# Kernel tuning notes

Hardware: AMD Instinct MI355X
Metric: run time of the kernel (lower is better)

The kernel has to match this reference:

```python
import jax, jax.numpy as jnp
import numpy as np
import math

EMBED = 1024
HEADS = 16
HEAD_DIM = EMBED // HEADS


def setup_inputs() -> dict:
    key = jax.random.key(0)
    ks = jax.random.split(key, 9)
    B, S = 2, 2048
    query = jax.random.normal(ks[0], (B, S, EMBED), dtype=jnp.float32)
    key_t = jax.random.normal(ks[1], (B, S, EMBED), dtype=jnp.float32)
    value = jax.random.normal(ks[2], (B, S, EMBED), dtype=jnp.float32)
    mask = jax.random.randint(ks[3], (B, 1, S, S), 0, 2, dtype=jnp.int32)
    # nn.Linear(head_dim, head_dim, bias=False) weights: [out, in]
    sc = 1.0 / math.sqrt(HEAD_DIM)
    Wq = jax.random.uniform(ks[4], (HEAD_DIM, HEAD_DIM), jnp.float32, -sc, sc)
    Wk = jax.random.uniform(ks[5], (HEAD_DIM, HEAD_DIM), jnp.float32, -sc, sc)
    Wv = jax.random.uniform(ks[6], (HEAD_DIM, HEAD_DIM), jnp.float32, -sc, sc)
    so = 1.0 / math.sqrt(EMBED)
    Wo = jax.random.uniform(ks[7], (EMBED, EMBED), jnp.float32, -so, so)
    bo = jax.random.uniform(ks[8], (EMBED,), jnp.float32, -so, so)
    return {"query": query, "key": key_t, "value": value, "mask": mask,
            "Wq": Wq, "Wk": Wk, "Wv": Wv, "Wo": Wo, "bo": bo}


def reference(query, key, value, mask, Wq, Wk, Wv, Wo, bo):
    B, Sq, E = query.shape
    Sk = key.shape[1]
    H, D = HEADS, HEAD_DIM
    # Faithful raw reshape into heads (as in the torch source, no transpose)
    q = query.reshape(B, H, Sq, D)
    k = key.reshape(B, H, Sk, D)
    v = value.reshape(B, H, Sk, D)
    # per-head_dim Linear (bias-free): x @ W.T
    Q = jnp.einsum('bhsd,ed->bhse', q, Wq)
    K = jnp.einsum('bhsd,ed->bhse', k, Wk)
    V = jnp.einsum('bhsd,ed->bhse', v, Wv)
    scores = jnp.einsum('bhqd,bhkd->bhqk', Q, K)  # [B,H,Sq,Sk]
    scores = jnp.where(mask == 0, jnp.float32(-1e20), scores)
    # NOTE: source divides by sqrt(embed_size), not sqrt(head_dim)
    attn = jax.nn.softmax(scores / jnp.float32(math.sqrt(E)), axis=-1)
    out = jnp.einsum('bhqk,bhkd->bhqd', attn, V).reshape(B, Sq, H * D)
    return out @ Wo.T + bo
```

## Files before the change

### kernel.cpp

```cpp
#include <hip/hip_runtime.h>

typedef __attribute__((ext_vector_type(8))) short short8;
typedef __attribute__((ext_vector_type(4))) float f32x4;
typedef __attribute__((ext_vector_type(2))) int int2v;
typedef __attribute__((ext_vector_type(4))) int int4v;

__device__ __forceinline__ short f2bf(float f) {
  unsigned u = __builtin_bit_cast(unsigned, f);
  u += 0x7fff + ((u >> 16) & 1);
  return (short)(u >> 16);
}

__device__ __forceinline__ int pk2bf(float lo, float hi) {
#if defined(__gfx950__) && __has_builtin(__builtin_amdgcn_cvt_pk_bf16_f32)
  typedef __attribute__((ext_vector_type(2))) __bf16 bf16x2;
  bf16x2 v = __builtin_amdgcn_cvt_pk_bf16_f32(lo, hi);
  return __builtin_bit_cast(int, v);
#else
  return (int)(unsigned short)(short)f2bf(lo) | (((int)f2bf(hi)) << 16);
#endif
}

__device__ __forceinline__ short8 pack8(f32x4 a, f32x4 b) {
  int4v t;
  t.x = pk2bf(a[0], a[1]);
  t.y = pk2bf(a[2], a[3]);
  t.z = pk2bf(b[0], b[1]);
  t.w = pk2bf(b[2], b[3]);
  return __builtin_bit_cast(short8, t);
}

__device__ __forceinline__ float fand(float p, int m) {
  return __builtin_bit_cast(float, __builtin_bit_cast(int, p) & m);
}

__device__ __forceinline__ float fexp2(float x) {
#if __has_builtin(__builtin_amdgcn_exp2f)
  return __builtin_amdgcn_exp2f(x);
#else
  return exp2f(x);
#endif
}

__device__ __forceinline__ float bf2f(short s) {
  return __builtin_bit_cast(float, ((int)(unsigned short)s) << 16);
}

__device__ __forceinline__ void glds16(const short* g, short* lbase, int lane) {
#if __has_builtin(__builtin_amdgcn_global_load_lds)
  __builtin_amdgcn_global_load_lds(
      (const __attribute__((address_space(1))) unsigned int*)g,
      (__attribute__((address_space(3))) unsigned int*)lbase, 16, 0, 0);
#else
  *(short8*)(lbase + lane * 8) = *(const short8*)g;
#endif
}

__global__ __launch_bounds__(256) void prep(const float* __restrict__ q,
                                            const float* __restrict__ k,
                                            const float* __restrict__ v,
                                            const float* __restrict__ Wq,
                                            const float* __restrict__ Wk,
                                            const float* __restrict__ Wv,
                                            const float* __restrict__ Wo,
                                            const int* __restrict__ mask,
                                            short* __restrict__ Qp,
                                            short* __restrict__ Kp,
                                            short* __restrict__ Vtp,
                                            short* __restrict__ Wob,
                                            unsigned* __restrict__ mmod) {
  const int bid = blockIdx.x;
  const int tid = threadIdx.x;

  if (bid >= 4096) {
    const int mb = bid - 4096;
    const int kp = mb & 15, bq = mb >> 4;
    const int b_ = bq >> 5, q64 = bq & 31;
    const int wv = tid >> 6, qd = (tid >> 4) & 3, m16_ = tid & 15;
    unsigned d = 0;
#pragma unroll
    for (int hb = 0; hb < 2; ++hb) {
      const int ka = kp * 2 + hb;
#pragma unroll
      for (int r = 0; r < 4; ++r) {
        const int* mr = mask + b_ * 4194304 +
                        (q64 * 64 + wv * 16 + qd * 4 + r) * 2048 + ka * 64 + m16_;
#pragma unroll
        for (int nt = 0; nt < 4; ++nt)
          if (mr[nt * 16] != 0) d |= 1u << (hb * 16 + r * 4 + nt);
      }
    }
    mmod[mb * 256 + tid] = d;
    return;
  }
  if (bid >= 3072) {
    const int i = ((bid - 3072) * 256 + tid) * 4;
    const f32x4 x = *(const f32x4*)&Wo[i];
    int2v o;
    o.x = pk2bf(x[0], x[1]);
    o.y = pk2bf(x[2], x[3]);
    *(int2v*)&Wob[i] = o;
    return;
  }

  __shared__ short xt[64][72];
  __shared__ short ot[64][72];
  const int mode = bid >> 10;
  const int bt = bid & 1023;
  const float* X;
  const float* W;
  float scale;
  if (mode == 0) { X = q; W = Wq; scale = 0.045084220f; }
  else if (mode == 1) { X = k; W = Wk; scale = 1.0f; }
  else { X = v; W = Wv; scale = 1.0f; }

  const int r0 = bt * 64;
  const int row = tid >> 2, seg = (tid & 3) * 16;
  const f32x4* xs = (const f32x4*)(X + (r0 + row) * 64 + seg);
  const f32x4 x0 = xs[0], x1 = xs[1], x2 = xs[2], x3 = xs[3];
  *(short8*)&xt[row][seg] = pack8(x0, x1);
  *(short8*)&xt[row][seg + 8] = pack8(x2, x3);
  __syncthreads();

  const int lane = tid & 63, wave = tid >> 6;
  const int m16 = lane & 15, quad = lane >> 4;

  const short8 a0 = *(const short8*)&xt[wave * 16 + m16][quad * 8];
  const short8 a1 = *(const short8*)&xt[wave * 16 + m16][32 + quad * 8];

  f32x4 acc[4];
#pragma unroll
  for (int nt = 0; nt < 4; ++nt) {
    const f32x4* wp0 = (const f32x4*)&W[(nt * 16 + m16) * 64 + quad * 8];
    const f32x4* wp1 = (const f32x4*)&W[(nt * 16 + m16) * 64 + 32 + quad * 8];
    const short8 b0 = pack8(wp0[0], wp0[1]);
    const short8 b1 = pack8(wp1[0], wp1[1]);
    f32x4 z = (f32x4){0.f, 0.f, 0.f, 0.f};
    z = __builtin_amdgcn_mfma_f32_16x16x32_bf16(a0, b0, z, 0, 0, 0);
    z = __builtin_amdgcn_mfma_f32_16x16x32_bf16(a1, b1, z, 0, 0, 0);
    acc[nt] = z;
  }

  if (mode != 2) {
#pragma unroll
    for (int nt = 0; nt < 4; ++nt)
#pragma unroll
      for (int r = 0; r < 4; ++r)
        ot[wave * 16 + quad * 4 + r][nt * 16 + m16] = f2bf(acc[nt][r] * scale);
  } else {
#pragma unroll
    for (int nt = 0; nt < 4; ++nt)
#pragma unroll
      for (int r = 0; r < 4; ++r)
        ot[nt * 16 + m16][16 * quad + 4 * r + wave] = f2bf(acc[nt][r]);
  }
  __syncthreads();

  const int orow = tid >> 2, opart = tid & 3;
  if (mode != 2) {
    short* dst = (mode == 0 ? Qp : Kp) + (r0 + orow) * 64 + opart * 16;
    *(short8*)&dst[0] = *(const short8*)&ot[orow][opart * 16];
    *(short8*)&dst[8] = *(const short8*)&ot[orow][opart * 16 + 8];
  } else {
    const int bh = r0 >> 11, s0 = r0 & 2047;
    short* dst = Vtp + bh * 131072 + orow * 2048 + s0 + opart * 16;
    *(short8*)&dst[0] = *(const short8*)&ot[orow][opart * 16];
    *(short8*)&dst[8] = *(const short8*)&ot[orow][opart * 16 + 8];
  }
}

__global__ __launch_bounds__(256, 4) void flash64s(const short* __restrict__ Qp,
                                                   const short* __restrict__ Kp,
                                                   const short* __restrict__ Vt,
                                                   const unsigned* __restrict__ mmod,
                                                   short* __restrict__ Opart,
                                                   float* __restrict__ lpart) {
  __shared__ __attribute__((aligned(16))) short kt[4096];
  __shared__ __attribute__((aligned(16))) short vt[4096];
  __shared__ __attribute__((aligned(16))) short pt[64][72];
  const int tid = threadIdx.x;
  const int bid = blockIdx.x;
  const int local = bid >> 3;
  const int khalf = local & 1;
  const int qblk = (local >> 1) & 31;
  const int bh = (bid & 7) * 4 + (local >> 6);
  const int q0 = qblk << 6;
  const int b = bh >> 4;
  const short* Qh = Qp + bh * 131072;
  const short* Kh = Kp + bh * 131072;
  const short* Vh = Vt + bh * 131072;
  const int lane = tid & 63, wave = tid >> 6;
  const int m16 = lane & 15, quad = lane >> 4;
  const int srow = lane >> 3, sj = (lane & 7) ^ srow;
  const int msh = m16 * 4;
  const int koff = m16 * 128 + ((quad ^ (m16 & 7)) * 16);

  const unsigned* mq = mmod + ((b * 32 + qblk) * 16 + khalf * 8) * 256 + tid;
  unsigned mw8[8];
#pragma unroll
  for (int kk = 0; kk < 8; ++kk) mw8[kk] = mq[kk * 256];

  short8 aq[2];
#pragma unroll
  for (int h = 0; h < 2; ++h)
    aq[h] = *(const short8*)&Qh[(q0 + wave * 16 + m16) * 64 + h * 32 + quad * 8];

  float l[4] = {0.f, 0.f, 0.f, 0.f};
  f32x4 oacc[4];
#pragma unroll
  for (int dt = 0; dt < 4; ++dt) oacc[dt] = (f32x4){0.f, 0.f, 0.f, 0.f};

  const int ka0 = khalf * 16;
  for (int kk = 0; kk < 8; ++kk) {
#pragma unroll
    for (int h = 0; h < 2; ++h) {
      const int ka = ka0 + kk * 2 + h;
      const int k0 = ka << 6;
      __syncthreads();
#pragma unroll
      for (int t = 0; t < 2; ++t) {
        const int crow = wave * 16 + t * 8;
        glds16(Kh + (ka * 64 + crow + srow) * 64 + sj * 8, kt + crow * 64, lane);
        glds16(Vh + (crow + srow) * 2048 + k0 + sj * 8, vt + crow * 64, lane);
      }
      __syncthreads();

      f32x4 s[4];
#pragma unroll
      for (int nt = 0; nt < 4; ++nt) {
        const int o0 = nt * 2048 + koff;
        const short8 kb0 = *(const short8*)((const char*)kt + o0);
        const short8 kb1 = *(const short8*)((const char*)kt + (o0 ^ 64));
        f32x4 z = (f32x4){0.f, 0.f, 0.f, 0.f};
        z = __builtin_amdgcn_mfma_f32_16x16x32_bf16(aq[0], kb0, z, 0, 0, 0);
        z = __builtin_amdgcn_mfma_f32_16x16x32_bf16(aq[1], kb1, z, 0, 0, 0);
        s[nt] = z;
      }

      const unsigned mw = mw8[kk];
      const int bitbase = h * 16;
#pragma unroll
      for (int r = 0; r < 4; ++r) {
        float p[4];
#pragma unroll
        for (int nt = 0; nt < 4; ++nt) {
          const int sh = 31 - (bitbase + r * 4 + nt);
          const int m = ((int)(mw << sh)) >> 31;
          p[nt] = fand(fexp2(s[nt][r]), m);
        }
        l[r] += (p[0] + p[1]) + (p[2] + p[3]);
        int2v pp;
        pp.x = pk2bf(p[0], p[1]);
        pp.y = pk2bf(p[2], p[3]);
        *(int2v*)&pt[wave * 16 + quad * 4 + r][msh] = pp;
      }

      const short8 ap0 = *(const short8*)&pt[wave * 16 + m16][quad * 8];
      const short8 ap1 = *(const short8*)&pt[wave * 16 + m16][32 + quad * 8];
#pragma unroll
      for (int dt = 0; dt < 4; ++dt) {
        const int o0 = dt * 2048 + koff;
        const short8 vb0 = *(const short8*)((const char*)vt + o0);
        const short8 vb1 = *(const short8*)((const char*)vt + (o0 ^ 64));
        f32x4 z = oacc[dt];
        z = __builtin_amdgcn_mfma_f32_16x16x32_bf16(ap0, vb0, z, 0, 0, 0);
        z = __builtin_amdgcn_mfma_f32_16x16x32_bf16(ap1, vb1, z, 0, 0, 0);
        oacc[dt] = z;
      }
    }
  }

  short* Oh = Opart + khalf * 4194304;
  float* lh = lpart + khalf * 65536;
#pragma unroll
  for (int r = 0; r < 4; ++r) {
#pragma unroll
    for (int off = 1; off < 16; off <<= 1) l[r] += __shfl_xor(l[r], off, 16);
    const float inv = 1.0f / l[r];
#pragma unroll
    for (int dt = 0; dt < 4; ++dt)
      pt[wave * 16 + quad * 4 + r][dt * 16 + m16] = f2bf(oacc[dt][r] * inv);
    if (m16 == 0) lh[bh * 2048 + q0 + wave * 16 + quad * 4 + r] = l[r];
  }

  const int orow = lane >> 2, opart = lane & 3;
  const int prow = wave * 16 + orow;
  short* og = Oh + (bh * 2048 + q0 + prow) * 64 + opart * 16;
  *(short8*)&og[0] = *(const short8*)&pt[prow][opart * 16];
  *(short8*)&og[8] = *(const short8*)&pt[prow][opart * 16 + 8];
}

__global__ __launch_bounds__(256) void outproj(const short* __restrict__ O0,
                                               const short* __restrict__ O1,
                                               const float* __restrict__ lp,
                                               const short* __restrict__ Wob,
                                               const float* __restrict__ bo,
                                               float* __restrict__ out) {
  __shared__ short at[64][72];
  __shared__ short bt[128][72];
  const int tid = threadIdx.x;
  const int bid = blockIdx.x;
  const int ct = bid >> 6, rt = bid & 63;
  const int r0 = rt * 64, c0 = ct * 128;
  const int lane = tid & 63, wave = tid >> 6;
  const int mr = (wave >> 1) * 32, nc = (wave & 1) * 64;
  const int m16 = lane & 15, quad = lane >> 4;
  const int arow = tid >> 2, apart = tid & 3;
  const int brow = tid >> 1, bhalf = (tid & 1) * 32;
  const int rr = r0 + arow;
  const int lbase = (rr >> 7) * 2048 + (rr & 127) * 16;

  f32x4 acc[2][4];
#pragma unroll
  for (int mt = 0; mt < 2; ++mt)
#pragma unroll
    for (int nt = 0; nt < 4; ++nt) acc[mt][nt] = (f32x4){0.f, 0.f, 0.f, 0.f};

  for (int kc = 0; kc < 16; ++kc) {
    const float l1 = lp[lbase + kc], l2 = lp[65536 + lbase + kc];
    const float is = 1.0f / (l1 + l2);
    const float w1 = l1 * is, w2 = l2 * is;
    const short8 a0 = *(const short8*)&O0[rr * 1024 + kc * 64 + apart * 16];
    const short8 a1 = *(const short8*)&O1[rr * 1024 + kc * 64 + apart * 16];
    const short8 a0b = *(const short8*)&O0[rr * 1024 + kc * 64 + apart * 16 + 8];
    const short8 a1b = *(const short8*)&O1[rr * 1024 + kc * 64 + apart * 16 + 8];
    const short* bg = &Wob[(c0 + brow) * 1024 + kc * 64 + bhalf];
    __syncthreads();
    int4v ca, cb;
    float f[8];
#pragma unroll
    for (int j = 0; j < 8; ++j) f[j] = w1 * bf2f(a0[j]) + w2 * bf2f(a1[j]);
    ca.x = pk2bf(f[0], f[1]); ca.y = pk2bf(f[2], f[3]);
    ca.z = pk2bf(f[4], f[5]); ca.w = pk2bf(f[6], f[7]);
#pragma unroll
    for (int j = 0; j < 8; ++j) f[j] = w1 * bf2f(a0b[j]) + w2 * bf2f(a1b[j]);
    cb.x = pk2bf(f[0], f[1]); cb.y = pk2bf(f[2], f[3]);
    cb.z = pk2bf(f[4], f[5]); cb.w = pk2bf(f[6], f[7]);
    *(short8*)&at[arow][apart * 16] = __builtin_bit_cast(short8, ca);
    *(short8*)&at[arow][apart * 16 + 8] = __builtin_bit_cast(short8, cb);
    *(short8*)&bt[brow][bhalf] = *(const short8*)&bg[0];
    *(short8*)&bt[brow][bhalf + 8] = *(const short8*)&bg[8];
    *(short8*)&bt[brow][bhalf + 16] = *(const short8*)&bg[16];
    *(short8*)&bt[brow][bhalf + 24] = *(const short8*)&bg[24];
    __syncthreads();

#pragma unroll
    for (int kh = 0; kh < 2; ++kh) {
      short8 af[2], bf[4];
#pragma unroll
      for (int i = 0; i < 2; ++i)
        af[i] = *(const short8*)&at[mr + i * 16 + m16][kh * 32 + quad * 8];
#pragma unroll
      for (int j = 0; j < 4; ++j)
        bf[j] = *(const short8*)&bt[nc + j * 16 + m16][kh * 32 + quad * 8];
#pragma unroll
      for (int mt = 0; mt < 2; ++mt)
#pragma unroll
        for (int nt = 0; nt < 4; ++nt)
          acc[mt][nt] = __builtin_amdgcn_mfma_f32_16x16x32_bf16(af[mt], bf[nt], acc[mt][nt], 0, 0, 0);
    }
  }

#pragma unroll
  for (int nt = 0; nt < 4; ++nt) {
    const int col = c0 + nc + nt * 16 + m16;
    const float bias = bo[col];
#pragma unroll
    for (int mt = 0; mt < 2; ++mt)
#pragma unroll
      for (int rr2 = 0; rr2 < 4; ++rr2)
        out[(r0 + mr + mt * 16 + quad * 4 + rr2) * 1024 + col] = acc[mt][nt][rr2] + bias;
  }
}

extern "C" void kernel_launch(void* const* d_in, const int* in_sizes, int n_in,
                              void* d_out, int out_size, void* d_ws, size_t ws_size,
                              hipStream_t stream) {
  const float* query = (const float*)d_in[0];
  const float* key = (const float*)d_in[1];
  const float* value = (const float*)d_in[2];
  const int* mask = (const int*)d_in[3];
  const float* Wq = (const float*)d_in[4];
  const float* Wk = (const float*)d_in[5];
  const float* Wv = (const float*)d_in[6];
  const float* Wo = (const float*)d_in[7];
  const float* bo = (const float*)d_in[8];
  float* out = (float*)d_out;

  char* ws = (char*)d_ws;
  short* Qp = (short*)(ws);
  short* Kp = (short*)(ws + 8388608);
  short* Vt = (short*)(ws + 16777216);
  short* Opart = (short*)(ws + 25165824);
  short* Wob = (short*)(ws + 41943040);
  float* lp = (float*)(ws + 44040192);
  unsigned* mmod = (unsigned*)(ws + 44564480);

  prep<<<5120, 256, 0, stream>>>(query, key, value, Wq, Wk, Wv, Wo, mask,
                                 Qp, Kp, Vt, Wob, mmod);
  flash64s<<<2048, 256, 0, stream>>>(Qp, Kp, Vt, mmod, Opart, lp);
  outproj<<<512, 256, 0, stream>>>(Opart, Opart + 4194304, lp, Wob, bo, out);
}
```

Baseline: 240.6 us.

## Enlarge flash attention query tile to 128 rows per block for K/V reuse

The attention kernel now handles 128 query rows per block, with each wave owning two 16-row groups, so every K/V tile staged in shared memory feeds twice as many MFMAs and the grid halves to 1024 blocks. The mask words and Q fragments are loaded per group. Probabilities are packed to bf16 by truncation instead of round-to-nearest, and the mask bit is extracted with a signed bitfield-extract builtin. The cost is roughly double the accumulator registers, which risks lower occupancy, fewer blocks to fill the GPU, and a small precision loss from truncating P.

```diff
diff --git a/kernel.cpp b/kernel.cpp
--- a/kernel.cpp
+++ b/kernel.cpp
@@ -21,6 +21,11 @@
 #endif
 }
 
+__device__ __forceinline__ int pktr(float lo, float hi) {
+  return (int)(__builtin_bit_cast(unsigned, lo) >> 16) |
+         (int)(__builtin_bit_cast(unsigned, hi) & 0xffff0000u);
+}
+
 __device__ __forceinline__ short8 pack8(f32x4 a, f32x4 b) {
   int4v t;
   t.x = pk2bf(a[0], a[1]);
@@ -32,6 +37,14 @@
 
 __device__ __forceinline__ float fand(float p, int m) {
   return __builtin_bit_cast(float, __builtin_bit_cast(int, p) & m);
+}
+
+__device__ __forceinline__ int bmask(unsigned w, int bit) {
+#if __has_builtin(__builtin_amdgcn_sbfe)
+  return __builtin_amdgcn_sbfe((int)w, bit, 1);
+#else
+  return ((int)(w << (31 - bit))) >> 31;
+#endif
 }
 
 __device__ __forceinline__ float fexp2(float x) {
@@ -169,22 +182,22 @@
   }
 }
 
-__global__ __launch_bounds__(256, 4) void flash64s(const short* __restrict__ Qp,
-                                                   const short* __restrict__ Kp,
-                                                   const short* __restrict__ Vt,
-                                                   const unsigned* __restrict__ mmod,
-                                                   short* __restrict__ Opart,
-                                                   float* __restrict__ lpart) {
+__global__ __launch_bounds__(256, 4) void flash128s(const short* __restrict__ Qp,
+                                                    const short* __restrict__ Kp,
+                                                    const short* __restrict__ Vt,
+                                                    const unsigned* __restrict__ mmod,
+                                                    short* __restrict__ Opart,
+                                                    float* __restrict__ lpart) {
   __shared__ __attribute__((aligned(16))) short kt[4096];
   __shared__ __attribute__((aligned(16))) short vt[4096];
-  __shared__ __attribute__((aligned(16))) short pt[64][72];
+  __shared__ __attribute__((aligned(16))) short pt[128][72];
   const int tid = threadIdx.x;
   const int bid = blockIdx.x;
   const int local = bid >> 3;
   const int khalf = local & 1;
-  const int qblk = (local >> 1) & 31;
-  const int bh = (bid & 7) * 4 + (local >> 6);
-  const int q0 = qblk << 6;
+  const int qblk = (local >> 1) & 15;
+  const int bh = (bid & 7) * 4 + (local >> 5);
+  const int q0 = qblk << 7;
   const int b = bh >> 4;
   const short* Qh = Qp + bh * 131072;
   const short* Kh = Kp + bh * 131072;
@@ -195,20 +208,34 @@
   const int msh = m16 * 4;
   const int koff = m16 * 128 + ((quad ^ (m16 & 7)) * 16);
 
-  const unsigned* mq = mmod + ((b * 32 + qblk) * 16 + khalf * 8) * 256 + tid;
-  unsigned mw8[8];
-#pragma unroll
-  for (int kk = 0; kk < 8; ++kk) mw8[kk] = mq[kk * 256];
-
-  short8 aq[2];
-#pragma unroll
-  for (int h = 0; h < 2; ++h)
-    aq[h] = *(const short8*)&Qh[(q0 + wave * 16 + m16) * 64 + h * 32 + quad * 8];
-
-  float l[4] = {0.f, 0.f, 0.f, 0.f};
-  f32x4 oacc[4];
-#pragma unroll
-  for (int dt = 0; dt < 4; ++dt) oacc[dt] = (f32x4){0.f, 0.f, 0.f, 0.f};
+  unsigned mw[2][8];
+#pragma unroll
+  for (int g = 0; g < 2; ++g) {
+    const int wg = 2 * wave + g;
+    const int q64 = 2 * qblk + (wg >> 2);
+    const int tidp = (wg & 3) * 64 + quad * 16 + m16;
+    const unsigned* mq = mmod + ((b * 32 + q64) * 16 + khalf * 8) * 256 + tidp;
+#pragma unroll
+    for (int kk = 0; kk < 8; ++kk) mw[g][kk] = mq[kk * 256];
+  }
+
+  short8 aq[2][2];
+#pragma unroll
+  for (int g = 0; g < 2; ++g)
+#pragma unroll
+    for (int h = 0; h < 2; ++h)
+      aq[g][h] = *(const short8*)&Qh[(q0 + wave * 32 + g * 16 + m16) * 64 + h * 32 + quad * 8];
+
+  float l[2][4];
+  f32x4 oacc[2][4];
+#pragma unroll
+  for (int g = 0; g < 2; ++g)
+#pragma unroll
+    for (int r = 0; r < 4; ++r) l[g][r] = 0.f;
+#pragma unroll
+  for (int g = 0; g < 2; ++g)
+#pragma unroll
+    for (int dt = 0; dt < 4; ++dt) oacc[g][dt] = (f32x4){0.f, 0.f, 0.f, 0.f};
 
   const int ka0 = khalf * 16;
   for (int kk = 0; kk < 8; ++kk) {
@@ -225,47 +252,58 @@
       }
       __syncthreads();
 
-      f32x4 s[4];
+      f32x4 s[2][4];
 #pragma unroll
       for (int nt = 0; nt < 4; ++nt) {
         const int o0 = nt * 2048 + koff;
         const short8 kb0 = *(const short8*)((const char*)kt + o0);
         const short8 kb1 = *(const short8*)((const char*)kt + (o0 ^ 64));
-        f32x4 z = (f32x4){0.f, 0.f, 0.f, 0.f};
-        z = __builtin_amdgcn_mfma_f32_16x16x32_bf16(aq[0], kb0, z, 0, 0, 0);
-        z = __builtin_amdgcn_mfma_f32_16x16x32_bf16(aq[1], kb1, z, 0, 0, 0);
-        s[nt] = z;
+#pragma unroll
+        for (int g = 0; g < 2; ++g) {
+          f32x4 z = (f32x4){0.f, 0.f, 0.f, 0.f};
+          z = __builtin_amdgcn_mfma_f32_16x16x32_bf16(aq[g][0], kb0, z, 0, 0, 0);
+          z = __builtin_amdgcn_mfma_f32_16x16x32_bf16(aq[g][1], kb1, z, 0, 0, 0);
+          s[g][nt] = z;
+        }
       }
 
-      const unsigned mw = mw8[kk];
       const int bitbase = h * 16;
 #pragma unroll
-      for (int r = 0; r < 4; ++r) {
-        float p[4];
-#pragma unroll
-        for (int nt = 0; nt < 4; ++nt) {
-          const int sh = 31 - (bitbase + r * 4 + nt);
-          const int m = ((int)(mw << sh)) >> 31;
-          p[nt] = fand(fexp2(s[nt][r]), m);
+      for (int g = 0; g < 2; ++g) {
+        const unsigned mg = mw[g][kk];
+#pragma unroll
+        for (int r = 0; r < 4; ++r) {
+          float p[4];
+#pragma unroll
+          for (int nt = 0; nt < 4; ++nt)
+            p[nt] = fand(fexp2(s[g][nt][r]), bmask(mg, bitbase + r * 4 + nt));
+          l[g][r] += (p[0] + p[1]) + (p[2] + p[3]);
+          int2v pp;
+          pp.x = pktr(p[0], p[1]);
+          pp.y = pktr(p[2], p[3]);
+          *(int2v*)&pt[wave * 32 + g * 16 + quad * 4 + r][msh] = pp;
         }
-        l[r] += (p[0] + p[1]) + (p[2] + p[3]);
-        int2v pp;
-        pp.x = pk2bf(p[0], p[1]);
-        pp.y = pk2bf(p[2], p[3]);
-        *(int2v*)&pt[wave * 16 + quad * 4 + r][msh] = pp;
       }
 
-      const short8 ap0 = *(const short8*)&pt[wave * 16 + m16][quad * 8];
-      const short8 ap1 = *(const short8*)&pt[wave * 16 + m16][32 + quad * 8];
+      short8 ap[2][2];
+#pragma unroll
+      for (int g = 0; g < 2; ++g)
+#pragma unroll
+        for (int hh = 0; hh < 2; ++hh)
+          ap[g][hh] = *(const short8*)&pt[wave * 32 + g * 16 + m16][hh * 32 + quad * 8];
+
 #pragma unroll
       for (int dt = 0; dt < 4; ++dt) {
         const int o0 = dt * 2048 + koff;
         const short8 vb0 = *(const short8*)((const char*)vt + o0);
         const short8 vb1 = *(const short8*)((const char*)vt + (o0 ^ 64));
-        f32x4 z = oacc[dt];
-        z = __builtin_amdgcn_mfma_f32_16x16x32_bf16(ap0, vb0, z, 0, 0, 0);
-        z = __builtin_amdgcn_mfma_f32_16x16x32_bf16(ap1, vb1, z, 0, 0, 0);
-        oacc[dt] = z;
+#pragma unroll
+        for (int g = 0; g < 2; ++g) {
+          f32x4 z = oacc[g][dt];
+          z = __builtin_amdgcn_mfma_f32_16x16x32_bf16(ap[g][0], vb0, z, 0, 0, 0);
+          z = __builtin_amdgcn_mfma_f32_16x16x32_bf16(ap[g][1], vb1, z, 0, 0, 0);
+          oacc[g][dt] = z;
+        }
       }
     }
   }
@@ -273,21 +311,24 @@
   short* Oh = Opart + khalf * 4194304;
   float* lh = lpart + khalf * 65536;
 #pragma unroll
-  for (int r = 0; r < 4; ++r) {
-#pragma unroll
-    for (int off = 1; off < 16; off <<= 1) l[r] += __shfl_xor(l[r], off, 16);
-    const float inv = 1.0f / l[r];
-#pragma unroll
-    for (int dt = 0; dt < 4; ++dt)
-      pt[wave * 16 + quad * 4 + r][dt * 16 + m16] = f2bf(oacc[dt][r] * inv);
-    if (m16 == 0) lh[bh * 2048 + q0 + wave * 16 + quad * 4 + r] = l[r];
-  }
-
-  const int orow = lane >> 2, opart = lane & 3;
-  const int prow = wave * 16 + orow;
-  short* og = Oh + (bh * 2048 + q0 + prow) * 64 + opart * 16;
-  *(short8*)&og[0] = *(const short8*)&pt[prow][opart * 16];
-  *(short8*)&og[8] = *(const short8*)&pt[prow][opart * 16 + 8];
+  for (int g = 0; g < 2; ++g)
+#pragma unroll
+    for (int r = 0; r < 4; ++r) {
+#pragma unroll
+      for (int off = 1; off < 16; off <<= 1) l[g][r] += __shfl_xor(l[g][r], off, 16);
+      const float inv = 1.0f / l[g][r];
+#pragma unroll
+      for (int dt = 0; dt < 4; ++dt)
+        pt[wave * 32 + g * 16 + quad * 4 + r][dt * 16 + m16] = f2bf(oacc[g][dt][r] * inv);
+      if (m16 == 0) lh[bh * 2048 + q0 + wave * 32 + g * 16 + quad * 4 + r] = l[g][r];
+    }
+
+  const int orow = lane >> 1, opart = lane & 1;
+  const int prow = wave * 32 + orow;
+  short* og = Oh + (bh * 2048 + q0 + prow) * 64 + opart * 32;
+#pragma unroll
+  for (int c = 0; c < 32; c += 8)
+    *(short8*)&og[c] = *(const short8*)&pt[prow][opart * 32 + c];
 }
 
 __global__ __launch_bounds__(256) void outproj(const short* __restrict__ O0,
@@ -398,6 +439,6 @@
 
   prep<<<5120, 256, 0, stream>>>(query, key, value, Wq, Wk, Wv, Wo, mask,
                                  Qp, Kp, Vt, Wob, mmod);
-  flash64s<<<2048, 256, 0, stream>>>(Qp, Kp, Vt, mmod, Opart, lp);
+  flash128s<<<1024, 256, 0, stream>>>(Qp, Kp, Vt, mmod, Opart, lp);
   outproj<<<512, 256, 0, stream>>>(Opart, Opart + 4194304, lp, Wob, bo, out);
 }
```

Result: slower. 301.4 us (+25.2%).

## Drop split-K attention partials; single-pass flash kernel writes normalized output directly

Applied to the files above, without the earlier changes.

The flash kernel no longer splits the key range into two halves. Each block now processes all 32 key tiles and writes a normalized bf16 output, so the out-projection kernel loads it directly instead of combining two partials weighted by row sums. Two smaller changes come with it: probabilities are packed to bf16 by truncation instead of round-to-nearest, and mask bits are extracted with sbfe. The grid halves to 1024 blocks with 4 waves each, which may reduce occupancy and latency hiding. In exchange it removes the partial-output traffic and the merge arithmetic.

```diff
diff --git a/kernel.cpp b/kernel.cpp
--- a/kernel.cpp
+++ b/kernel.cpp
@@ -21,6 +21,11 @@
 #endif
 }
 
+__device__ __forceinline__ int pktr(float lo, float hi) {
+  return (int)(__builtin_bit_cast(unsigned, lo) >> 16) |
+         (int)(__builtin_bit_cast(unsigned, hi) & 0xffff0000u);
+}
+
 __device__ __forceinline__ short8 pack8(f32x4 a, f32x4 b) {
   int4v t;
   t.x = pk2bf(a[0], a[1]);
@@ -34,16 +39,20 @@
   return __builtin_bit_cast(float, __builtin_bit_cast(int, p) & m);
 }
 
+__device__ __forceinline__ int bmask(unsigned w, int bit) {
+#if __has_builtin(__builtin_amdgcn_sbfe)
+  return __builtin_amdgcn_sbfe((int)w, bit, 1);
+#else
+  return ((int)(w << (31 - bit))) >> 31;
+#endif
+}
+
 __device__ __forceinline__ float fexp2(float x) {
 #if __has_builtin(__builtin_amdgcn_exp2f)
   return __builtin_amdgcn_exp2f(x);
 #else
   return exp2f(x);
 #endif
-}
-
-__device__ __forceinline__ float bf2f(short s) {
-  return __builtin_bit_cast(float, ((int)(unsigned short)s) << 16);
 }
 
 __device__ __forceinline__ void glds16(const short* g, short* lbase, int lane) {
@@ -169,21 +178,19 @@
   }
 }
 
-__global__ __launch_bounds__(256, 4) void flash64s(const short* __restrict__ Qp,
-                                                   const short* __restrict__ Kp,
-                                                   const short* __restrict__ Vt,
-                                                   const unsigned* __restrict__ mmod,
-                                                   short* __restrict__ Opart,
-                                                   float* __restrict__ lpart) {
+__global__ __launch_bounds__(256) void flash64f(const short* __restrict__ Qp,
+                                                const short* __restrict__ Kp,
+                                                const short* __restrict__ Vt,
+                                                const unsigned* __restrict__ mmod,
+                                                short* __restrict__ Ob) {
   __shared__ __attribute__((aligned(16))) short kt[4096];
   __shared__ __attribute__((aligned(16))) short vt[4096];
   __shared__ __attribute__((aligned(16))) short pt[64][72];
   const int tid = threadIdx.x;
   const int bid = blockIdx.x;
   const int local = bid >> 3;
-  const int khalf = local & 1;
-  const int qblk = (local >> 1) & 31;
-  const int bh = (bid & 7) * 4 + (local >> 6);
+  const int qblk = local & 31;
+  const int bh = (bid & 7) * 4 + (local >> 5);
   const int q0 = qblk << 6;
   const int b = bh >> 4;
   const short* Qh = Qp + bh * 131072;
@@ -194,11 +201,7 @@
   const int srow = lane >> 3, sj = (lane & 7) ^ srow;
   const int msh = m16 * 4;
   const int koff = m16 * 128 + ((quad ^ (m16 & 7)) * 16);
-
-  const unsigned* mq = mmod + ((b * 32 + qblk) * 16 + khalf * 8) * 256 + tid;
-  unsigned mw8[8];
-#pragma unroll
-  for (int kk = 0; kk < 8; ++kk) mw8[kk] = mq[kk * 256];
+  const unsigned* mq = mmod + ((b * 32 + qblk) * 16) * 256 + tid;
 
   short8 aq[2];
 #pragma unroll
@@ -210,11 +213,11 @@
 #pragma unroll
   for (int dt = 0; dt < 4; ++dt) oacc[dt] = (f32x4){0.f, 0.f, 0.f, 0.f};
 
-  const int ka0 = khalf * 16;
-  for (int kk = 0; kk < 8; ++kk) {
+  for (int kk = 0; kk < 16; ++kk) {
+    const unsigned mw = mq[kk * 256];
 #pragma unroll
     for (int h = 0; h < 2; ++h) {
-      const int ka = ka0 + kk * 2 + h;
+      const int ka = kk * 2 + h;
       const int k0 = ka << 6;
       __syncthreads();
 #pragma unroll
@@ -237,21 +240,17 @@
         s[nt] = z;
       }
 
-      const unsigned mw = mw8[kk];
       const int bitbase = h * 16;
 #pragma unroll
       for (int r = 0; r < 4; ++r) {
         float p[4];
 #pragma unroll
-        for (int nt = 0; nt < 4; ++nt) {
-          const int sh = 31 - (bitbase + r * 4 + nt);
-          const int m = ((int)(mw << sh)) >> 31;
-          p[nt] = fand(fexp2(s[nt][r]), m);
-        }
+        for (int nt = 0; nt < 4; ++nt)
+          p[nt] = fand(fexp2(s[nt][r]), bmask(mw, bitbase + r * 4 + nt));
         l[r] += (p[0] + p[1]) + (p[2] + p[3]);
         int2v pp;
-        pp.x = pk2bf(p[0], p[1]);
-        pp.y = pk2bf(p[2], p[3]);
+        pp.x = pktr(p[0], p[1]);
+        pp.y = pktr(p[2], p[3]);
         *(int2v*)&pt[wave * 16 + quad * 4 + r][msh] = pp;
       }
 
@@ -270,8 +269,6 @@
     }
   }
 
-  short* Oh = Opart + khalf * 4194304;
-  float* lh = lpart + khalf * 65536;
 #pragma unroll
   for (int r = 0; r < 4; ++r) {
 #pragma unroll
@@ -280,19 +277,16 @@
 #pragma unroll
     for (int dt = 0; dt < 4; ++dt)
       pt[wave * 16 + quad * 4 + r][dt * 16 + m16] = f2bf(oacc[dt][r] * inv);
-    if (m16 == 0) lh[bh * 2048 + q0 + wave * 16 + quad * 4 + r] = l[r];
   }
 
   const int orow = lane >> 2, opart = lane & 3;
   const int prow = wave * 16 + orow;
-  short* og = Oh + (bh * 2048 + q0 + prow) * 64 + opart * 16;
+  short* og = Ob + (bh * 2048 + q0 + prow) * 64 + opart * 16;
   *(short8*)&og[0] = *(const short8*)&pt[prow][opart * 16];
   *(short8*)&og[8] = *(const short8*)&pt[prow][opart * 16 + 8];
 }
 
-__global__ __launch_bounds__(256) void outproj(const short* __restrict__ O0,
-                                               const short* __restrict__ O1,
-                                               const float* __restrict__ lp,
+__global__ __launch_bounds__(256) void outproj(const short* __restrict__ Ob,
                                                const short* __restrict__ Wob,
                                                const float* __restrict__ bo,
                                                float* __restrict__ out) {
@@ -307,8 +301,6 @@
   const int m16 = lane & 15, quad = lane >> 4;
   const int arow = tid >> 2, apart = tid & 3;
   const int brow = tid >> 1, bhalf = (tid & 1) * 32;
-  const int rr = r0 + arow;
-  const int lbase = (rr >> 7) * 2048 + (rr & 127) * 16;
 
   f32x4 acc[2][4];
 #pragma unroll
@@ -317,27 +309,11 @@
     for (int nt = 0; nt < 4; ++nt) acc[mt][nt] = (f32x4){0.f, 0.f, 0.f, 0.f};
 
   for (int kc = 0; kc < 16; ++kc) {
-    const float l1 = lp[lbase + kc], l2 = lp[65536 + lbase + kc];
-    const float is = 1.0f / (l1 + l2);
-    const float w1 = l1 * is, w2 = l2 * is;
-    const short8 a0 = *(const short8*)&O0[rr * 1024 + kc * 64 + apart * 16];
-    const short8 a1 = *(const short8*)&O1[rr * 1024 + kc * 64 + apart * 16];
-    const short8 a0b = *(const short8*)&O0[rr * 1024 + kc * 64 + apart * 16 + 8];
-    const short8 a1b = *(const short8*)&O1[rr * 1024 + kc * 64 + apart * 16 + 8];
+    __syncthreads();
+    const short* ag = &Ob[(r0 + arow) * 1024 + kc * 64 + apart * 16];
     const short* bg = &Wob[(c0 + brow) * 1024 + kc * 64 + bhalf];
-    __syncthreads();
-    int4v ca, cb;
-    float f[8];
-#pragma unroll
-    for (int j = 0; j < 8; ++j) f[j] = w1 * bf2f(a0[j]) + w2 * bf2f(a1[j]);
-    ca.x = pk2bf(f[0], f[1]); ca.y = pk2bf(f[2], f[3]);
-    ca.z = pk2bf(f[4], f[5]); ca.w = pk2bf(f[6], f[7]);
-#pragma unroll
-    for (int j = 0; j < 8; ++j) f[j] = w1 * bf2f(a0b[j]) + w2 * bf2f(a1b[j]);
-    cb.x = pk2bf(f[0], f[1]); cb.y = pk2bf(f[2], f[3]);
-    cb.z = pk2bf(f[4], f[5]); cb.w = pk2bf(f[6], f[7]);
-    *(short8*)&at[arow][apart * 16] = __builtin_bit_cast(short8, ca);
-    *(short8*)&at[arow][apart * 16 + 8] = __builtin_bit_cast(short8, cb);
+    *(short8*)&at[arow][apart * 16] = *(const short8*)&ag[0];
+    *(short8*)&at[arow][apart * 16 + 8] = *(const short8*)&ag[8];
     *(short8*)&bt[brow][bhalf] = *(const short8*)&bg[0];
     *(short8*)&bt[brow][bhalf + 8] = *(const short8*)&bg[8];
     *(short8*)&bt[brow][bhalf + 16] = *(const short8*)&bg[16];
@@ -391,13 +367,12 @@
   short* Qp = (short*)(ws);
   short* Kp = (short*)(ws + 8388608);
   short* Vt = (short*)(ws + 16777216);
-  short* Opart = (short*)(ws + 25165824);
+  short* Ob = (short*)(ws + 25165824);
   short* Wob = (short*)(ws + 41943040);
-  float* lp = (float*)(ws + 44040192);
   unsigned* mmod = (unsigned*)(ws + 44564480);
 
   prep<<<5120, 256, 0, stream>>>(query, key, value, Wq, Wk, Wv, Wo, mask,
                                  Qp, Kp, Vt, Wob, mmod);
-  flash64s<<<2048, 256, 0, stream>>>(Qp, Kp, Vt, mmod, Opart, lp);
-  outproj<<<512, 256, 0, stream>>>(Opart, Opart + 4194304, lp, Wob, bo, out);
-}
+  flash64f<<<1024, 256, 0, stream>>>(Qp, Kp, Vt, mmod, Ob);
+  outproj<<<512, 256, 0, stream>>>(Ob, Wob, bo, out);
+}
```

After: 238.7 us. No clear change (-0.8%).
